# Kernel optimization log

Hardware: AMD Instinct MI355X
Metric: run time of the kernel (lower is better)

The kernel has to match this reference:

```python
import jax, jax.numpy as jnp
import numpy as np

K = 7  # kernel_size


def setup_inputs() -> dict:
    key = jax.random.key(0)
    ks = jax.random.split(key, 7)
    B, C, H, W = 32, 256, 56, 56
    x = jax.random.normal(ks[0], (B, C, H, W), jnp.float32)
    # BatchNorm2d affine params
    bn_gamma = 1.0 + 0.1 * jax.random.normal(ks[1], (C,), jnp.float32)
    bn_beta = 0.1 * jax.random.normal(ks[2], (C,), jnp.float32)
    # Linear(k^2 -> k), torch weight layout (out, in)
    w0 = jax.random.normal(ks[3], (K, K * K), jnp.float32) / np.sqrt(K * K)
    # LayerNorm([C, k]) affine params
    ln_gamma = 1.0 + 0.1 * jax.random.normal(ks[4], (C, K), jnp.float32)
    ln_beta = 0.1 * jax.random.normal(ks[5], (C, K), jnp.float32)
    # Linear(k -> k^2)
    w1 = jax.random.normal(ks[6], (K * K, K), jnp.float32) / np.sqrt(K)
    return dict(x=x, bn_gamma=bn_gamma, bn_beta=bn_beta, w0=w0,
                ln_gamma=ln_gamma, ln_beta=ln_beta, w1=w1)


def reference(x, bn_gamma, bn_beta, w0, ln_gamma, ln_beta, w1):
    B, C, H, W = x.shape
    k = K
    eps = 1e-5
    # AdaptiveAvgPool2d((k,k)); H,W divisible by k -> exact block means
    p = x.reshape(B, C, k, H // k, k, W // k).mean(axis=(3, 5))  # (B,C,k,k)
    # BatchNorm2d (training-mode batch statistics, biased variance)
    mu = p.mean(axis=(0, 2, 3), keepdims=True)
    var = p.var(axis=(0, 2, 3), keepdims=True)
    p = (p - mu) * jax.lax.rsqrt(var + eps)
    p = p * bn_gamma[None, :, None, None] + bn_beta[None, :, None, None]
    # b c kh kw -> b c (kh kw), then Linear(k^2 -> k)
    v = p.reshape(B, C, k * k) @ w0.T  # (B,C,k)
    # LayerNorm over the (C,k) normalized shape
    m = v.mean(axis=(1, 2), keepdims=True)
    s = v.var(axis=(1, 2), keepdims=True)
    v = (v - m) * jax.lax.rsqrt(s + eps) * ln_gamma[None] + ln_beta[None]
    v = jax.nn.sigmoid(v)
    v = v @ w1.T  # (B,C,k^2)
    kern = v.reshape(B * C, 1, k, k)  # per-sample, per-channel depthwise kernels
    # F.conv2d(groups=B*C, padding='same', stride=1); odd k -> 'SAME' matches torch
    out = jax.lax.conv_general_dilated(
        x.reshape(1, B * C, H, W), kern,
        window_strides=(1, 1), padding='SAME',
        feature_group_count=B * C,
        dimension_numbers=('NCHW', 'OIHW', 'NCHW'))
    return out.reshape(B, C, H, W)
```

## Files before the change

kernel.cpp:

```cpp
#include <hip/hip_runtime.h>
#include <math.h>

#define BATCH 32
#define CH    256
#define HH    56
#define WW    56
#define HW    3136
#define KS    7
#define KK    49
#define NIMG  8192
#define TPITCH 62
#define TROWS  20
#define TSIZE  (TPITCH * TROWS)

__global__ __launch_bounds__(256) void pool_kernel(const float* __restrict__ x,
                                                   float* __restrict__ p,
                                                   float2* __restrict__ ss) {
    __shared__ float cells[4][KK];
    const int t = threadIdx.x;
    const int wid = t >> 6, lane = t & 63;
    const int img = blockIdx.x * 4 + wid;
    float* cw = cells[wid];
    if (lane < KK) cw[lane] = 0.f;
    asm volatile("s_waitcnt lgkmcnt(0)" ::: "memory");
    __builtin_amdgcn_wave_barrier();
    const float4* xp = (const float4*)(x + (size_t)img * HW);
    #pragma unroll
    for (int k = 0; k < 13; ++k) {
        const int j = k * 64 + lane;
        if (j < 784) {
            const float4 v = xp[j];
            const int r = j / 14, q = j - r * 14;
            atomicAdd(&cw[(r >> 3) * KS + (q >> 1)], (v.x + v.y) + (v.z + v.w));
        }
    }
    asm volatile("s_waitcnt lgkmcnt(0)" ::: "memory");
    __builtin_amdgcn_wave_barrier();
    float v = 0.f;
    if (lane < KK) {
        v = cw[lane] * (1.0f / 64.0f);
        p[(size_t)img * KK + lane] = v;
    }
    float v2 = v * v;
    #pragma unroll
    for (int o = 32; o >= 1; o >>= 1) {
        v  += __shfl_down(v,  o, 64);
        v2 += __shfl_down(v2, o, 64);
    }
    if (lane == 0) ss[img] = make_float2(v, v2);
}

__global__ __launch_bounds__(256) void mid_kernel(const float* __restrict__ p,
                                                  const float2* __restrict__ ss,
                                                  const float* __restrict__ bng,
                                                  const float* __restrict__ bnb,
                                                  const float* __restrict__ w0,
                                                  const float* __restrict__ lng,
                                                  const float* __restrict__ lnb,
                                                  const float* __restrict__ w1,
                                                  float* __restrict__ ker) {
    const int b = blockIdx.x, c = threadIdx.x;
    __shared__ float s_w0[KS * KK], s_w1[KK * KS];
    __shared__ float r1[4], r2[4];
    for (int i = c; i < KS * KK; i += 256) { s_w0[i] = w0[i]; s_w1[i] = w1[i]; }
    float S = 0.f, S2 = 0.f;
    #pragma unroll 4
    for (int bb = 0; bb < BATCH; ++bb) {
        const float2 t2 = ss[(size_t)bb * CH + c];
        S += t2.x; S2 += t2.y;
    }
    {
        const float inv  = 1.0f / (float)(BATCH * KK);
        const float mu   = S * inv;
        const float var  = S2 * inv - mu * mu;
        const float rstd = rsqrtf(var + 1e-5f);
        S  = bng[c] * rstd;
        S2 = bnb[c] - mu * S;
    }
    __syncthreads();
    float pn[KK];
    const float* pp = p + ((size_t)b * CH + c) * KK;
    #pragma unroll
    for (int i = 0; i < KK; ++i) pn[i] = pp[i] * S + S2;
    float v[KS];
    float ls = 0.f, ls2 = 0.f;
    #pragma unroll
    for (int j = 0; j < KS; ++j) {
        float a = 0.f;
        #pragma unroll
        for (int i = 0; i < KK; ++i) a += pn[i] * s_w0[j * KK + i];
        v[j] = a; ls += a; ls2 += a * a;
    }
    #pragma unroll
    for (int o = 32; o >= 1; o >>= 1) {
        ls  += __shfl_down(ls, o, 64);
        ls2 += __shfl_down(ls2, o, 64);
    }
    const int w = threadIdx.x >> 6;
    if ((threadIdx.x & 63) == 0) { r1[w] = ls; r2[w] = ls2; }
    __syncthreads();
    const float Sv  = r1[0] + r1[1] + r1[2] + r1[3];
    const float Sv2 = r2[0] + r2[1] + r2[2] + r2[3];
    const float inv = 1.0f / (float)(CH * KS);
    const float m   = Sv * inv;
    const float var = Sv2 * inv - m * m;
    const float rs  = rsqrtf(var + 1e-5f);
    float sg[KS];
    #pragma unroll
    for (int j = 0; j < KS; ++j) {
        const float vn = (v[j] - m) * rs * lng[c * KS + j] + lnb[c * KS + j];
        sg[j] = 1.0f / (1.0f + expf(-vn));
    }
    float* ko = ker + ((size_t)b * CH + c) * KK;
    #pragma unroll
    for (int i = 0; i < KK; ++i) {
        float a = 0.f;
        #pragma unroll
        for (int j = 0; j < KS; ++j) a += sg[j] * s_w1[i * KS + j];
        ko[i] = a;
    }
}

__global__ __launch_bounds__(256, 6) void conv_kernel(const float* __restrict__ x,
                                                      const float* __restrict__ ker,
                                                      float* __restrict__ out) {
    __shared__ float tile[4 * TSIZE];
    const int t = threadIdx.x;
    const int wid = t >> 6, lane = t & 63;
    const int img = blockIdx.x;
    const int r0 = wid * 14;
    float* tl = tile + wid * TSIZE;
    const float* kp = ker + (size_t)img * KK;
    float tap[KK];
    #pragma unroll
    for (int i = 0; i < KK; ++i)
        tap[i] = __int_as_float(__builtin_amdgcn_readfirstlane(__float_as_int(kp[i])));
    const float* xi = x + (size_t)img * HW;
    #pragma unroll
    for (int rr = 0; rr < TROWS; ++rr) {
        const int g = r0 + rr - 3;
        if (lane < 56) {
            float v = 0.f;
            if ((unsigned)g < 56u) v = xi[g * WW + lane];
            tl[rr * TPITCH + lane + 3] = v;
        } else {
            const int j = lane - 56;
            if (j < 6) tl[rr * TPITCH + ((j < 3) ? j : 56 + j)] = 0.f;
        }
    }
    asm volatile("s_waitcnt lgkmcnt(0)" ::: "memory");
    __builtin_amdgcn_wave_barrier();
    const int cc = (lane < 56) ? lane : 55;
    float acc[14];
    #pragma unroll
    for (int o = 0; o < 14; ++o) acc[o] = 0.f;
    #pragma unroll
    for (int rr = 0; rr < TROWS; ++rr) {
        float w[KS];
        #pragma unroll
        for (int kw = 0; kw < KS; ++kw) w[kw] = tl[rr * TPITCH + cc + kw];
        #pragma unroll
        for (int kr = 0; kr < KS; ++kr) {
            const int o = rr - kr;
            if (o < 0 || o > 13) continue;
            #pragma unroll
            for (int kw = 0; kw < KS; ++kw)
                acc[o] += w[kw] * tap[kr * KS + kw];
        }
    }
    if (lane < 56) {
        float* oi = out + (size_t)img * HW;
        #pragma unroll
        for (int o = 0; o < 14; ++o)
            oi[(r0 + o) * WW + lane] = acc[o];
    }
}

extern "C" void kernel_launch(void* const* d_in, const int* in_sizes, int n_in,
                              void* d_out, int out_size, void* d_ws, size_t ws_size,
                              hipStream_t stream) {
    const float* x   = (const float*)d_in[0];
    const float* bng = (const float*)d_in[1];
    const float* bnb = (const float*)d_in[2];
    const float* w0  = (const float*)d_in[3];
    const float* lng = (const float*)d_in[4];
    const float* lnb = (const float*)d_in[5];
    const float* w1  = (const float*)d_in[6];
    float* out = (float*)d_out;

    float* ws   = (float*)d_ws;
    float* p    = ws;
    float* kern = p + (size_t)NIMG * KK;
    float2* ss  = (float2*)d_out;

    hipLaunchKernelGGL(pool_kernel, dim3(NIMG / 4), dim3(256), 0, stream, x, p, ss);
    hipLaunchKernelGGL(mid_kernel,  dim3(BATCH),    dim3(256), 0, stream, p, ss,
                       bng, bnb, w0, lng, lnb, w1, kern);
    hipLaunchKernelGGL(conv_kernel, dim3(NIMG),     dim3(256), 0, stream, x, kern, out);
}
```

Measured before the change: 262.0 us.

## Replace pool atomics with shuffle reductions, transpose pooled layout, double-buffer conv rows

The pool kernel drops LDS atomics: each lane accumulates row sums in registers and reduces them with cross-lane shuffles. It also stores pooled values channel-major (cell-major across images), so mid_kernel's loads become coalesced across threads. The conv kernel software-pipelines LDS row loads with ping-pong register buffers and lowers the launch-bounds occupancy hint from 6 to 4, trading occupancy for more registers. Fully unrolled code raises register pressure.

```diff
diff --git a/kernel.cpp b/kernel.cpp
--- a/kernel.cpp
+++ b/kernel.cpp
@@ -16,32 +16,33 @@
 __global__ __launch_bounds__(256) void pool_kernel(const float* __restrict__ x,
                                                    float* __restrict__ p,
                                                    float2* __restrict__ ss) {
-    __shared__ float cells[4][KK];
-    const int t = threadIdx.x;
-    const int wid = t >> 6, lane = t & 63;
+    const int t = threadIdx.x, wid = t >> 6, lane = t & 63;
     const int img = blockIdx.x * 4 + wid;
-    float* cw = cells[wid];
-    if (lane < KK) cw[lane] = 0.f;
-    asm volatile("s_waitcnt lgkmcnt(0)" ::: "memory");
-    __builtin_amdgcn_wave_barrier();
     const float4* xp = (const float4*)(x + (size_t)img * HW);
-    #pragma unroll
-    for (int k = 0; k < 13; ++k) {
-        const int j = k * 64 + lane;
-        if (j < 784) {
-            const float4 v = xp[j];
-            const int r = j / 14, q = j - r * 14;
-            atomicAdd(&cw[(r >> 3) * KS + (q >> 1)], (v.x + v.y) + (v.z + v.w));
+    float s[7] = {0.f, 0.f, 0.f, 0.f, 0.f, 0.f, 0.f};
+    if (lane < 56) {
+        #pragma unroll
+        for (int i = 0; i < 14; ++i) {
+            const float4 v = xp[i * 56 + lane];
+            s[i >> 1] += (v.x + v.y) + (v.z + v.w);
         }
     }
-    asm volatile("s_waitcnt lgkmcnt(0)" ::: "memory");
-    __builtin_amdgcn_wave_barrier();
-    float v = 0.f;
-    if (lane < KK) {
-        v = cw[lane] * (1.0f / 64.0f);
-        p[(size_t)img * KK + lane] = v;
-    }
-    float v2 = v * v;
+    #pragma unroll
+    for (int c = 0; c < 7; ++c) {
+        s[c] += __shfl(s[c], lane + 28, 64);
+        s[c] += __shfl(s[c], lane + 14, 64);
+        s[c] += __shfl(s[c], lane + 1,  64);
+        s[c] *= (1.0f / 64.0f);
+    }
+    const bool owner = (lane < 14) && !(lane & 1);
+    const int cq = lane >> 1;
+    float v = 0.f, v2 = 0.f;
+    #pragma unroll
+    for (int c = 0; c < 7; ++c) {
+        if (owner) p[((size_t)(c * KS + cq)) * NIMG + img] = s[c];
+        v += s[c]; v2 += s[c] * s[c];
+    }
+    if (!owner) { v = 0.f; v2 = 0.f; }
     #pragma unroll
     for (int o = 32; o >= 1; o >>= 1) {
         v  += __shfl_down(v,  o, 64);
@@ -79,9 +80,10 @@
     }
     __syncthreads();
     float pn[KK];
-    const float* pp = p + ((size_t)b * CH + c) * KK;
-    #pragma unroll
-    for (int i = 0; i < KK; ++i) pn[i] = pp[i] * S + S2;
+    const size_t base = (size_t)b * CH + c;
+    #pragma unroll
+    for (int i = 0; i < KK; ++i)
+        pn[i] = p[(size_t)i * NIMG + base] * S + S2;
     float v[KS];
     float ls = 0.f, ls2 = 0.f;
     #pragma unroll
@@ -111,7 +113,7 @@
         const float vn = (v[j] - m) * rs * lng[c * KS + j] + lnb[c * KS + j];
         sg[j] = 1.0f / (1.0f + expf(-vn));
     }
-    float* ko = ker + ((size_t)b * CH + c) * KK;
+    float* ko = ker + base * KK;
     #pragma unroll
     for (int i = 0; i < KK; ++i) {
         float a = 0.f;
@@ -121,7 +123,7 @@
     }
 }
 
-__global__ __launch_bounds__(256, 6) void conv_kernel(const float* __restrict__ x,
+__global__ __launch_bounds__(256, 4) void conv_kernel(const float* __restrict__ x,
                                                       const float* __restrict__ ker,
                                                       float* __restrict__ out) {
     __shared__ float tile[4 * TSIZE];
@@ -154,20 +156,31 @@
     float acc[14];
     #pragma unroll
     for (int o = 0; o < 14; ++o) acc[o] = 0.f;
-    #pragma unroll
-    for (int rr = 0; rr < TROWS; ++rr) {
-        float w[KS];
-        #pragma unroll
-        for (int kw = 0; kw < KS; ++kw) w[kw] = tl[rr * TPITCH + cc + kw];
-        #pragma unroll
-        for (int kr = 0; kr < KS; ++kr) {
-            const int o = rr - kr;
-            if (o < 0 || o > 13) continue;
-            #pragma unroll
-            for (int kw = 0; kw < KS; ++kw)
-                acc[o] += w[kw] * tap[kr * KS + kw];
-        }
-    }
+
+    float wA[KS], wB[KS];
+    #define LDROW(RR, W)                                        \
+        {   const int _b = (RR) * TPITCH + cc;                  \
+            _Pragma("unroll")                                   \
+            for (int kw = 0; kw < KS; ++kw) W[kw] = tl[_b + kw]; }
+    #define FMAROW(RR, W)                                       \
+        {   _Pragma("unroll")                                   \
+            for (int kr = 0; kr < KS; ++kr) {                   \
+                const int o = (RR) - kr;                        \
+                if (o >= 0 && o <= 13) {                        \
+                    _Pragma("unroll")                           \
+                    for (int kw = 0; kw < KS; ++kw)             \
+                        acc[o] += W[kw] * tap[kr * KS + kw];    \
+                } } }
+    LDROW(0, wA);
+    #pragma unroll
+    for (int rr = 0; rr < TROWS; rr += 2) {
+        if (rr + 1 < TROWS) LDROW(rr + 1, wB);
+        FMAROW(rr, wA);
+        if (rr + 2 < TROWS) LDROW(rr + 2, wA);
+        if (rr + 1 < TROWS) FMAROW(rr + 1, wB);
+    }
+    #undef LDROW
+    #undef FMAROW
     if (lane < 56) {
         float* oi = out + (size_t)img * HW;
         #pragma unroll
```

Result: faster. 256.1 us (-2.3%).
